# Performance work log

Measured on AMD Instinct MI355X. Metric: run time of the kernel, lower is better.

## Reference

```python
import jax, jax.numpy as jnp
import numpy as np

B, T, FEAT, H, E, NT, NH = 64, 256, 188, 512, 1024, 14, 8
HD = E // NH  # head dim = 128


def _gru_dir(x, w_ih, w_hh, b_ih, b_hh):
    # x: [T, B, in]; PyTorch GRU gate order: r, z, n
    xp = jnp.einsum('tbi,gi->tbg', x, w_ih) + b_ih  # [T,B,3H]

    def step(h, xt):
        hp = h @ w_hh.T + b_hh
        r = jax.nn.sigmoid(xt[..., :H] + hp[..., :H])
        z = jax.nn.sigmoid(xt[..., H:2 * H] + hp[..., H:2 * H])
        n = jnp.tanh(xt[..., 2 * H:] + r * hp[..., 2 * H:])
        h = (1 - z) * n + z * h
        return h, h

    h0 = jnp.zeros((x.shape[1], H), x.dtype)
    _, hs = jax.lax.scan(step, h0, xp)
    return hs  # [T,B,H]


def _bigru(x, wf, wb):
    f = _gru_dir(x, *wf)
    b = _gru_dir(x[::-1], *wb)[::-1]
    return jnp.concatenate([f, b], -1)  # [T,B,2H]


def _forward(features, ne_table, g1f, g1b, g2f, g2b, q_w, q_b, k_w, k_b, v_w, v_b,
             out_w, out_b, lin_w, lin_b, crf_start, crf_end, crf_trans, labels):
    nb = features.shape[0]
    x = features.transpose(1, 0, 2)  # [T,B,FEAT]
    enc = _bigru(x, g1f, g1b)        # [T,B,2H]=[T,B,E]
    # NE embedding: arange(14) rows for every batch element -> [S=14, B, 14]
    ne = jnp.broadcast_to(ne_table[:, None, :], (NT, nb, NT))
    # nn.MultiheadAttention with kdim=vdim=NT
    q = (enc @ q_w.T + q_b).reshape(T, nb, NH, HD)
    k = (ne @ k_w.T + k_b).reshape(NT, nb, NH, HD)
    v = (ne @ v_w.T + v_b).reshape(NT, nb, NH, HD)
    scores = jnp.einsum('tbhd,sbhd->bhts', q, k) / jnp.sqrt(jnp.float32(HD))
    attn = jax.nn.softmax(scores, axis=-1)
    ao = jnp.einsum('bhts,sbhd->tbhd', attn, v).reshape(T, nb, E)
    ao = ao @ out_w.T + out_b
    dec_in = jnp.concatenate([enc, ao], -1)   # [T,B,4H]
    dec = _bigru(dec_in, g2f, g2b)            # [T,B,2H]
    dec = dec @ lin_w.T + lin_b               # [T,B,NT]
    dec = dec.transpose(1, 0, 2)              # [B,T,NT]
    # scaled dot product against NE embeddings -> emissions [B,T,NT]
    logits = jnp.einsum('btd,sd->bts', dec, ne_table) / jnp.sqrt(jnp.float32(NT))
    # CRF negative log likelihood, reduction='mean', full mask
    em = jnp.take_along_axis(logits, labels[..., None], axis=2)[..., 0]  # [B,T]
    num = (crf_start[labels[:, 0]] + em.sum(1)
           + crf_trans[labels[:, :-1], labels[:, 1:]].sum(1)
           + crf_end[labels[:, -1]])
    alpha0 = crf_start + logits[:, 0]  # [B,NT]

    def step(a, e_t):
        a = jax.nn.logsumexp(a[:, :, None] + crf_trans[None] + e_t[:, None, :], axis=1)
        return a, None

    alpha, _ = jax.lax.scan(step, alpha0, logits[:, 1:].transpose(1, 0, 2))
    den = jax.nn.logsumexp(alpha + crf_end, axis=1)
    return -(num - den).mean()


def setup_inputs() -> dict:
    key = jax.random.key(0)
    ks = iter(jax.random.split(key, 40))

    def rn(shape, s=0.05):
        return jax.random.normal(next(ks), shape, jnp.float32) * s

    inp = {}
    inp['features'] = jax.random.normal(next(ks), (B, T, FEAT), jnp.float32)
    inp['labels'] = jax.random.randint(next(ks), (B, T), 0, NT)
    inp['ne_table'] = rn((NT, NT), 0.5).at[0].set(0.0)  # padding_idx=0
    for g, fi in (('gru1', FEAT), ('gru2', 4 * H)):
        for d in ('f', 'b'):
            inp[f'{g}_w_ih_{d}'] = rn((3 * H, fi))
            inp[f'{g}_w_hh_{d}'] = rn((3 * H, H))
            inp[f'{g}_b_ih_{d}'] = rn((3 * H,))
            inp[f'{g}_b_hh_{d}'] = rn((3 * H,))
    inp['q_w'] = rn((E, E)); inp['q_b'] = rn((E,))
    inp['k_w'] = rn((E, NT)); inp['k_b'] = rn((E,))
    inp['v_w'] = rn((E, NT)); inp['v_b'] = rn((E,))
    inp['out_w'] = rn((E, E)); inp['out_b'] = rn((E,))
    inp['lin_w'] = rn((NT, 2 * H)); inp['lin_b'] = rn((NT,))
    inp['crf_start'] = rn((NT,), 0.1)
    inp['crf_end'] = rn((NT,), 0.1)
    inp['crf_trans'] = rn((NT, NT), 0.1)
    return inp


def reference(features, labels, ne_table,
              gru1_w_ih_f, gru1_w_hh_f, gru1_b_ih_f, gru1_b_hh_f,
              gru1_w_ih_b, gru1_w_hh_b, gru1_b_ih_b, gru1_b_hh_b,
              gru2_w_ih_f, gru2_w_hh_f, gru2_b_ih_f, gru2_b_hh_f,
              gru2_w_ih_b, gru2_w_hh_b, gru2_b_ih_b, gru2_b_hh_b,
              q_w, q_b, k_w, k_b, v_w, v_b, out_w, out_b,
              lin_w, lin_b, crf_start, crf_end, crf_trans):
    return _forward(features, ne_table,
                    (gru1_w_ih_f, gru1_w_hh_f, gru1_b_ih_f, gru1_b_hh_f),
                    (gru1_w_ih_b, gru1_w_hh_b, gru1_b_ih_b, gru1_b_hh_b),
                    (gru2_w_ih_f, gru2_w_hh_f, gru2_b_ih_f, gru2_b_hh_f),
                    (gru2_w_ih_b, gru2_w_hh_b, gru2_b_ih_b, gru2_b_hh_b),
                    q_w, q_b, k_w, k_b, v_w, v_b, out_w, out_b,
                    lin_w, lin_b, crf_start, crf_end, crf_trans, labels)
```

## Files before the change

kernel.cpp:

```cpp
#include <hip/hip_runtime.h>
#include <hip/hip_bf16.h>
#include <math.h>

typedef __hip_bfloat16 bf16;
typedef __bf16 bf16x8 __attribute__((ext_vector_type(8)));
typedef float  f32x4  __attribute__((ext_vector_type(4)));
typedef unsigned long long u64;

#define T_SEQ 256
#define BATCH 64
#define FEATD 188
#define HID   512
#define EMB   1024
#define NTAG  14
#define G3    1536
#define GRU_NBLK 32
#define DIR_NBLK 16

__global__ __launch_bounds__(256) void f32_to_bf16(
    const float* __restrict__ src, bf16* __restrict__ dst, int n4)
{
  int i = blockIdx.x * 256 + threadIdx.x;
  if (i >= n4) return;
  float4 v = *(const float4*)(src + (size_t)i * 4);
  bf16 o[4] = {__float2bfloat16(v.x), __float2bfloat16(v.y),
               __float2bfloat16(v.z), __float2bfloat16(v.w)};
  *(ushort4*)(dst + (size_t)i * 4) = *(ushort4*)o;
}

__global__ __launch_bounds__(256) void gemm_mfma(
    const bf16* __restrict__ A1, int lda1,
    const bf16* __restrict__ A2, int lda2, int K1,
    const bf16* __restrict__ W, int ldw,
    const float* __restrict__ bias,
    bf16* __restrict__ C, int ldc,
    int M, int N, int K)
{
  __shared__ __bf16 As[128][40];
  __shared__ __bf16 Bs[128][40];
  const int bm = blockIdx.y * 128;
  const int bn = blockIdx.x * 128;
  const int tid = threadIdx.x;
  const int wave = tid >> 6, lane = tid & 63;
  const int wr = wave >> 1, wc = wave & 1;
  const int lr = lane & 15, lk = (lane >> 4) << 3;
  f32x4 acc[4][4] = {};
  for (int k0 = 0; k0 < K; k0 += 32) {
#pragma unroll
    for (int p = 0; p < 4; ++p) {
      int i = tid + p * 256;
      int row = i >> 3, q = i & 7;
      int kg = k0 + q * 4;
      ushort4 va{0, 0, 0, 0}, vb{0, 0, 0, 0};
      if (kg < K) {
        const bf16* srca = (kg < K1) ? A1 + (size_t)(bm + row) * lda1 + kg
                                     : A2 + (size_t)(bm + row) * lda2 + (kg - K1);
        va = *(const ushort4*)srca;
        vb = *(const ushort4*)(W + (size_t)(bn + row) * ldw + kg);
      }
      *(ushort4*)&As[row][q * 4] = va;
      *(ushort4*)&Bs[row][q * 4] = vb;
    }
    __syncthreads();
    bf16x8 af[4], bf_[4];
#pragma unroll
    for (int i = 0; i < 4; ++i)
      af[i] = *(const bf16x8*)&As[wr * 64 + i * 16 + lr][lk];
#pragma unroll
    for (int j = 0; j < 4; ++j)
      bf_[j] = *(const bf16x8*)&Bs[wc * 64 + j * 16 + lr][lk];
#pragma unroll
    for (int i = 0; i < 4; ++i)
#pragma unroll
      for (int j = 0; j < 4; ++j)
        acc[i][j] = __builtin_amdgcn_mfma_f32_16x16x32_bf16(af[i], bf_[j], acc[i][j], 0, 0, 0);
    __syncthreads();
  }
#pragma unroll
  for (int j = 0; j < 4; ++j) {
    int n = bn + wc * 64 + j * 16 + lr;
    float bv = bias ? bias[n] : 0.f;
#pragma unroll
    for (int i = 0; i < 4; ++i) {
#pragma unroll
      for (int p = 0; p < 4; ++p) {
        int m = bm + wr * 64 + i * 16 + (lane >> 4) * 4 + p;
        C[(size_t)m * ldc + n] = __float2bfloat16(acc[i][j][p] + bv);
      }
    }
  }
}

__global__ __launch_bounds__(256) void transpose_feat(
    const float* __restrict__ f, bf16* __restrict__ xT)
{
  const int idx = blockIdx.x * 256 + threadIdx.x;
  const int total = BATCH * T_SEQ * FEATD;
  if (idx >= total) return;
  const int i = idx % FEATD;
  const int r = idx / FEATD;
  const int b = r / T_SEQ;
  const int t = r % T_SEQ;
  xT[((size_t)t * BATCH + b) * FEATD + i] = __float2bfloat16(f[idx]);
}

__global__ __launch_bounds__(256, 1) void gru_persist(
    const bf16* __restrict__ xp_f, const bf16* __restrict__ xp_b,
    const bf16* __restrict__ whh_f, const bf16* __restrict__ whh_b,
    const float* __restrict__ bhh_f, const float* __restrict__ bhh_b,
    bf16* __restrict__ out, int* __restrict__ cnt)
{
  const int blk = blockIdx.x;
  const int dir = blk >> 4;
  const int ct  = blk & 15;
  const bf16* xp   = dir ? xp_b  : xp_f;
  const bf16* whh  = dir ? whh_b : whh_f;
  const float* bhh = dir ? bhh_b : bhh_f;
  const int off = dir ? HID : 0;
  const int tid = threadIdx.x;
  const int wave = tid >> 6, lane = tid & 63;
  const int lr = lane & 15, lkq = lane >> 4;
  int* mycnt = cnt + dir * T_SEQ;

  __shared__ __bf16 Ws[96][520];
  __shared__ __bf16 Hst[2][64][36];
  for (int i = tid; i < 96 * 64; i += 256) {
    int r = i >> 6, q = i & 63;
    int grow = (r >> 5) * HID + ct * 32 + (r & 31);
    *(float4*)&Ws[r][q * 8] = *(const float4*)(whh + (size_t)grow * HID + q * 8);
  }
  __syncthreads();

  float bh[3][2];
#pragma unroll
  for (int g = 0; g < 3; ++g)
#pragma unroll
    for (int nf = 0; nf < 2; ++nf)
      bh[g][nf] = bhh[g * HID + ct * 32 + nf * 16 + lr];

  bf16 xc[3][2][4];
  {
    const int t0 = dir ? (T_SEQ - 1) : 0;
    const size_t xbase = (size_t)t0 * BATCH * G3;
#pragma unroll
    for (int p = 0; p < 4; ++p) {
      const size_t xrow = xbase + (size_t)(wave * 16 + lkq * 4 + p) * G3;
#pragma unroll
      for (int g = 0; g < 3; ++g)
#pragma unroll
        for (int nf = 0; nf < 2; ++nf)
          xc[g][nf][p] = xp[xrow + g * HID + ct * 32 + nf * 16 + lr];
    }
  }

  for (int s = 0; s < T_SEQ; ++s) {
    const int t = dir ? (T_SEQ - 1 - s) : s;
    const int cur = s & 1, prv = cur ^ 1;

    f32x4 acc[3][2] = {};
    if (s > 0) {
      const bf16* arow = out + (size_t)(dir ? t + 1 : t - 1) * BATCH * EMB + off
                         + (size_t)(wave * 16 + lr) * EMB + lkq * 8;
      union { u64 v[2]; bf16x8 f; } hb[16];
#pragma unroll
      for (int ki = 0; ki < 16; ++ki) {
        hb[ki].v[0] = __hip_atomic_load((const u64*)(arow + ki * 32),
                                        __ATOMIC_RELAXED, __HIP_MEMORY_SCOPE_AGENT);
        hb[ki].v[1] = __hip_atomic_load((const u64*)(arow + ki * 32 + 4),
                                        __ATOMIC_RELAXED, __HIP_MEMORY_SCOPE_AGENT);
      }
#pragma unroll
      for (int ki = 0; ki < 16; ++ki) {
#pragma unroll
        for (int g = 0; g < 3; ++g)
#pragma unroll
          for (int nf = 0; nf < 2; ++nf) {
            bf16x8 b = *(const bf16x8*)&Ws[g * 32 + nf * 16 + lr][ki * 32 + lkq * 8];
            acc[g][nf] = __builtin_amdgcn_mfma_f32_16x16x32_bf16(hb[ki].f, b, acc[g][nf], 0, 0, 0);
          }
      }
    }

#pragma unroll
    for (int nf = 0; nf < 2; ++nf) {
      const int cl = nf * 16 + lr;
#pragma unroll
      for (int p = 0; p < 4; ++p) {
        const int m = wave * 16 + lkq * 4 + p;
        float hp = (s > 0) ? (float)Hst[prv][m][cl] : 0.f;
        float xr = __bfloat162float(xc[0][nf][p]);
        float xz = __bfloat162float(xc[1][nf][p]);
        float xn = __bfloat162float(xc[2][nf][p]);
        float r = 1.f / (1.f + expf(-(xr + acc[0][nf][p] + bh[0][nf])));
        float z = 1.f / (1.f + expf(-(xz + acc[1][nf][p] + bh[1][nf])));
        float n = tanhf(xn + r * (acc[2][nf][p] + bh[2][nf]));
        Hst[cur][m][cl] = (__bf16)((1.f - z) * n + z * hp);
      }
    }
    __syncthreads();

    const size_t obase = (size_t)t * BATCH * EMB + off + ct * 32;
    for (int i = tid; i < 512; i += 256) {
      int row = i >> 3, qq = i & 7;
      u64 v = *(const u64*)&Hst[cur][row][qq * 4];
      __hip_atomic_store((u64*)(out + obase + (size_t)row * EMB + qq * 4), v,
                         __ATOMIC_RELAXED, __HIP_MEMORY_SCOPE_AGENT);
    }
    asm volatile("s_waitcnt vmcnt(0)" ::: "memory");
    __syncthreads();

    if (tid == 0)
      __hip_atomic_fetch_add(&mycnt[s], 1, __ATOMIC_RELAXED, __HIP_MEMORY_SCOPE_AGENT);

    if (s + 1 < T_SEQ) {
      const int tn = dir ? (T_SEQ - 2 - s) : (s + 1);
      const size_t xb2 = (size_t)tn * BATCH * G3;
#pragma unroll
      for (int p = 0; p < 4; ++p) {
        const size_t xrow = xb2 + (size_t)(wave * 16 + lkq * 4 + p) * G3;
#pragma unroll
        for (int g = 0; g < 3; ++g)
#pragma unroll
          for (int nf = 0; nf < 2; ++nf)
            xc[g][nf][p] = xp[xrow + g * HID + ct * 32 + nf * 16 + lr];
      }
    }

    if (tid == 0) {
      while (__hip_atomic_load(&mycnt[s], __ATOMIC_RELAXED, __HIP_MEMORY_SCOPE_AGENT) < DIR_NBLK)
        __builtin_amdgcn_s_sleep(1);
    }
    __syncthreads();
  }
}

__global__ __launch_bounds__(256) void kv_kernel(
    const float* __restrict__ ne, const float* __restrict__ k_w,
    const float* __restrict__ k_b, const float* __restrict__ v_w,
    const float* __restrict__ v_b, float* __restrict__ kk,
    float* __restrict__ vv)
{
  const int e = blockIdx.x * 256 + threadIdx.x;
  if (e >= EMB) return;
#pragma unroll
  for (int s = 0; s < NTAG; ++s) {
    float a = k_b[e], c = v_b[e];
#pragma unroll
    for (int i = 0; i < NTAG; ++i) {
      float nv = ne[s * NTAG + i];
      a = fmaf(nv, k_w[e * NTAG + i], a);
      c = fmaf(nv, v_w[e * NTAG + i], c);
    }
    kk[s * EMB + e] = a;
    vv[s * EMB + e] = c;
  }
}

__global__ __launch_bounds__(256) void attn_kernel(
    const bf16* __restrict__ q, const float* __restrict__ kk,
    const float* __restrict__ vv, bf16* __restrict__ ao)
{
  const int unit = blockIdx.x * 4 + (threadIdx.x >> 6);
  const int h = unit & 7;
  const int tb = unit >> 3;
  const int lane = threadIdx.x & 63;
  const size_t qbase = (size_t)tb * EMB + h * 128;
  const int kbase = h * 128 + lane;
  float q0 = __bfloat162float(q[qbase + lane]);
  float q1 = __bfloat162float(q[qbase + 64 + lane]);
  float sc[NTAG];
#pragma unroll
  for (int j = 0; j < NTAG; ++j) {
    float p = q0 * kk[j * EMB + kbase] + q1 * kk[j * EMB + 64 + kbase];
#pragma unroll
    for (int d = 32; d; d >>= 1) p += __shfl_xor(p, d);
    sc[j] = p * 0.088388347648318447f;
  }
  float m = sc[0];
#pragma unroll
  for (int j = 1; j < NTAG; ++j) m = fmaxf(m, sc[j]);
  float sum = 0.f;
#pragma unroll
  for (int j = 0; j < NTAG; ++j) { sc[j] = expf(sc[j] - m); sum += sc[j]; }
  float inv = 1.f / sum;
  float o0 = 0.f, o1 = 0.f;
#pragma unroll
  for (int j = 0; j < NTAG; ++j) {
    float p = sc[j] * inv;
    o0 = fmaf(p, vv[j * EMB + kbase], o0);
    o1 = fmaf(p, vv[j * EMB + 64 + kbase], o1);
  }
  ao[qbase + lane] = __float2bfloat16(o0);
  ao[qbase + 64 + lane] = __float2bfloat16(o1);
}

__global__ __launch_bounds__(256) void dec_logits_kernel(
    const bf16* __restrict__ dec, const float* __restrict__ lin_w,
    const float* __restrict__ lin_b, const float* __restrict__ ne,
    float* __restrict__ logits)
{
  const int tb = blockIdx.x * 4 + (threadIdx.x >> 6);
  const int t = tb >> 6;
  const int b = tb & 63;
  const int lane = threadIdx.x & 63;
  const bf16* drow = dec + (size_t)tb * EMB;
  float dv[16];
#pragma unroll
  for (int i = 0; i < 16; ++i) dv[i] = __bfloat162float(drow[lane + 64 * i]);
  float dl[NTAG];
#pragma unroll
  for (int n = 0; n < NTAG; ++n) {
    float p = 0.f;
#pragma unroll
    for (int i = 0; i < 16; ++i)
      p = fmaf(dv[i], lin_w[n * EMB + lane + 64 * i], p);
#pragma unroll
    for (int d = 32; d; d >>= 1) p += __shfl_xor(p, d);
    dl[n] = p + lin_b[n];
  }
  if (lane < NTAG) {
    float acc = 0.f;
#pragma unroll
    for (int d2 = 0; d2 < NTAG; ++d2)
      acc = fmaf(dl[d2], ne[lane * NTAG + d2], acc);
    logits[((size_t)b * T_SEQ + t) * NTAG + lane] = acc * 0.26726124191242439f;
  }
}

__global__ __launch_bounds__(64) void crf_kernel(
    const float* __restrict__ logits, const int* __restrict__ labels,
    const float* __restrict__ cstart, const float* __restrict__ cend,
    const float* __restrict__ ctrans, float* __restrict__ lossb)
{
  const int b = blockIdx.x;
  const int lane = threadIdx.x;
  __shared__ float al[NTAG];
  __shared__ float tr[NTAG * NTAG];
  __shared__ float tmp[NTAG];
  const float* lg = logits + (size_t)b * T_SEQ * NTAG;
  const int* lab = labels + (size_t)b * T_SEQ;
  for (int i = lane; i < NTAG * NTAG; i += 64) tr[i] = ctrans[i];
  if (lane < NTAG) al[lane] = cstart[lane] + lg[lane];
  __syncthreads();
  for (int t = 1; t < T_SEQ; ++t) {
    float v = 0.f;
    if (lane < NTAG) {
      float mx = -1e30f;
#pragma unroll
      for (int i = 0; i < NTAG; ++i) mx = fmaxf(mx, al[i] + tr[i * NTAG + lane]);
      float sm = 0.f;
#pragma unroll
      for (int i = 0; i < NTAG; ++i) sm += expf(al[i] + tr[i * NTAG + lane] - mx);
      v = mx + logf(sm) + lg[t * NTAG + lane];
    }
    __syncthreads();
    if (lane < NTAG) al[lane] = v;
    __syncthreads();
  }
  float em = 0.f;
  for (int t = lane; t < T_SEQ; t += 64) em += lg[t * NTAG + lab[t]];
  float trs = 0.f;
  for (int t = lane; t < T_SEQ - 1; t += 64) trs += tr[lab[t] * NTAG + lab[t + 1]];
  float p = em + trs;
#pragma unroll
  for (int d = 32; d; d >>= 1) p += __shfl_xor(p, d);
  if (lane < NTAG) tmp[lane] = al[lane] + cend[lane];
  __syncthreads();
  if (lane == 0) {
    float num = p + cstart[lab[0]] + cend[lab[T_SEQ - 1]];
    float mx = tmp[0];
#pragma unroll
    for (int i = 1; i < NTAG; ++i) mx = fmaxf(mx, tmp[i]);
    float sm = 0.f;
#pragma unroll
    for (int i = 0; i < NTAG; ++i) sm += expf(tmp[i] - mx);
    float den = mx + logf(sm);
    lossb[b] = -(num - den);
  }
}

__global__ __launch_bounds__(64) void final_reduce(
    const float* __restrict__ lossb, float* __restrict__ out)
{
  float v = lossb[threadIdx.x];
#pragma unroll
  for (int d = 32; d; d >>= 1) v += __shfl_xor(v, d);
  if (threadIdx.x == 0) out[0] = v * (1.f / 64.f);
}

extern "C" void kernel_launch(void* const* d_in, const int* in_sizes, int n_in,
                              void* d_out, int out_size, void* d_ws, size_t ws_size,
                              hipStream_t stream)
{
  const float* features = (const float*)d_in[0];
  const int*   labels   = (const int*)d_in[1];
  const float* ne_table = (const float*)d_in[2];
  const float* g1_wih_f = (const float*)d_in[3];
  const float* g1_whh_f = (const float*)d_in[4];
  const float* g1_bih_f = (const float*)d_in[5];
  const float* g1_bhh_f = (const float*)d_in[6];
  const float* g1_wih_b = (const float*)d_in[7];
  const float* g1_whh_b = (const float*)d_in[8];
  const float* g1_bih_b = (const float*)d_in[9];
  const float* g1_bhh_b = (const float*)d_in[10];
  const float* g2_wih_f = (const float*)d_in[11];
  const float* g2_whh_f = (const float*)d_in[12];
  const float* g2_bih_f = (const float*)d_in[13];
  const float* g2_bhh_f = (const float*)d_in[14];
  const float* g2_wih_b = (const float*)d_in[15];
  const float* g2_whh_b = (const float*)d_in[16];
  const float* g2_bih_b = (const float*)d_in[17];
  const float* g2_bhh_b = (const float*)d_in[18];
  const float* q_w   = (const float*)d_in[19];
  const float* q_b   = (const float*)d_in[20];
  const float* k_w   = (const float*)d_in[21];
  const float* k_b   = (const float*)d_in[22];
  const float* v_w   = (const float*)d_in[23];
  const float* v_b   = (const float*)d_in[24];
  const float* out_w = (const float*)d_in[25];
  const float* out_b = (const float*)d_in[26];
  const float* lin_w = (const float*)d_in[27];
  const float* lin_b = (const float*)d_in[28];
  const float* crf_start = (const float*)d_in[29];
  const float* crf_end   = (const float*)d_in[30];
  const float* crf_trans = (const float*)d_in[31];

  const size_t NTB = (size_t)T_SEQ * BATCH;
  char* base = (char*)d_ws;
  size_t off = 0;
  auto alloc = [&](size_t bytes) {
    char* p = base + off;
    off += (bytes + 255) & ~(size_t)255;
    return p;
  };
  bf16* xpA  = (bf16*)alloc(NTB * G3 * sizeof(bf16));
  bf16* xpB  = (bf16*)alloc(NTB * G3 * sizeof(bf16));
  bf16* enc  = (bf16*)alloc(NTB * EMB * sizeof(bf16));
  bf16* bufD = (bf16*)alloc(NTB * EMB * sizeof(bf16));
  bf16* bufE = (bf16*)alloc(NTB * EMB * sizeof(bf16));
  float* kkbuf  = (float*)alloc((size_t)NTAG * EMB * sizeof(float));
  float* vvbuf  = (float*)alloc((size_t)NTAG * EMB * sizeof(float));
  float* logits = (float*)alloc(NTB * NTAG * sizeof(float));
  float* lossb  = (float*)alloc(64 * sizeof(float));
  int*   bcnt   = (int*)alloc(1024 * sizeof(int));
  bf16* w1if = (bf16*)alloc((size_t)G3 * FEATD * sizeof(bf16));
  bf16* w1ib = (bf16*)alloc((size_t)G3 * FEATD * sizeof(bf16));
  bf16* w1hf = (bf16*)alloc((size_t)G3 * HID * sizeof(bf16));
  bf16* w1hb = (bf16*)alloc((size_t)G3 * HID * sizeof(bf16));
  bf16* w2if = (bf16*)alloc((size_t)G3 * 2 * EMB * sizeof(bf16));
  bf16* w2ib = (bf16*)alloc((size_t)G3 * 2 * EMB * sizeof(bf16));
  bf16* w2hf = (bf16*)alloc((size_t)G3 * HID * sizeof(bf16));
  bf16* w2hb = (bf16*)alloc((size_t)G3 * HID * sizeof(bf16));
  bf16* wq   = (bf16*)alloc((size_t)EMB * EMB * sizeof(bf16));
  bf16* wo   = (bf16*)alloc((size_t)EMB * EMB * sizeof(bf16));
  (void)off; (void)ws_size; (void)in_sizes; (void)n_in; (void)out_size;

  bf16* xT = bufD;

  const int M = (int)NTB;
  dim3 blk(256);

  hipMemsetAsync(bcnt, 0, 1024 * sizeof(int), stream);

  auto conv = [&](const float* s, bf16* d, size_t n) {
    f32_to_bf16<<<(int)((n / 4 + 255) / 256), blk, 0, stream>>>(s, d, (int)(n / 4));
  };
  conv(g1_wih_f, w1if, (size_t)G3 * FEATD);
  conv(g1_wih_b, w1ib, (size_t)G3 * FEATD);
  conv(g1_whh_f, w1hf, (size_t)G3 * HID);
  conv(g1_whh_b, w1hb, (size_t)G3 * HID);
  conv(g2_wih_f, w2if, (size_t)G3 * 2 * EMB);
  conv(g2_wih_b, w2ib, (size_t)G3 * 2 * EMB);
  conv(g2_whh_f, w2hf, (size_t)G3 * HID);
  conv(g2_whh_b, w2hb, (size_t)G3 * HID);
  conv(q_w, wq, (size_t)EMB * EMB);
  conv(out_w, wo, (size_t)EMB * EMB);

  transpose_feat<<<(BATCH * T_SEQ * FEATD + 255) / 256, blk, 0, stream>>>(features, xT);

  dim3 g_xp(G3 / 128, M / 128);
  dim3 g_e(EMB / 128, M / 128);

  gemm_mfma<<<g_xp, blk, 0, stream>>>(xT, FEATD, nullptr, 0, FEATD,
                                      w1if, FEATD, g1_bih_f, xpA, G3, M, G3, FEATD);
  gemm_mfma<<<g_xp, blk, 0, stream>>>(xT, FEATD, nullptr, 0, FEATD,
                                      w1ib, FEATD, g1_bih_b, xpB, G3, M, G3, FEATD);

  gru_persist<<<GRU_NBLK, blk, 0, stream>>>(xpA, xpB, w1hf, w1hb,
                                            g1_bhh_f, g1_bhh_b, enc, bcnt);

  kv_kernel<<<4, blk, 0, stream>>>(ne_table, k_w, k_b, v_w, v_b, kkbuf, vvbuf);
  gemm_mfma<<<g_e, blk, 0, stream>>>(enc, EMB, nullptr, 0, EMB,
                                     wq, EMB, q_b, bufE, EMB, M, EMB, EMB);

  attn_kernel<<<M * 2, blk, 0, stream>>>(bufE, kkbuf, vvbuf, bufD);
  gemm_mfma<<<g_e, blk, 0, stream>>>(bufD, EMB, nullptr, 0, EMB,
                                     wo, EMB, out_b, bufE, EMB, M, EMB, EMB);

  gemm_mfma<<<g_xp, blk, 0, stream>>>(enc, EMB, bufE, EMB, EMB,
                                      w2if, 2 * EMB, g2_bih_f, xpA, G3, M, G3, 2 * EMB);
  gemm_mfma<<<g_xp, blk, 0, stream>>>(enc, EMB, bufE, EMB, EMB,
                                      w2ib, 2 * EMB, g2_bih_b, xpB, G3, M, G3, 2 * EMB);

  gru_persist<<<GRU_NBLK, blk, 0, stream>>>(xpA, xpB, w2hf, w2hb,
                                            g2_bhh_f, g2_bhh_b, bufD, bcnt + 512);

  dec_logits_kernel<<<M / 4, blk, 0, stream>>>(bufD, lin_w, lin_b, ne_table, logits);

  crf_kernel<<<BATCH, 64, 0, stream>>>(logits, labels, crf_start, crf_end, crf_trans, lossb);
  final_reduce<<<1, 64, 0, stream>>>(lossb, (float*)d_out);
}
```

Before: 5.042 ms.

## Restructure persistent GRU: register-resident weights, fewer blocks, per-block flag barrier

The persistent GRU kernel now runs 8 blocks per direction instead of 16, and each wave keeps its slice of the recurrent weights in registers rather than LDS. Each step stages the full previous hidden state into swizzled LDS and computes 64 gate columns per block. The hidden state stays in fp32 registers, and outputs are written as packed bf16 pairs straight from the accumulators. The old atomic counter barrier, polled by one thread followed by __syncthreads, is replaced by per-block ready flags that a whole wave polls. This shortens the inter-block synchronisation latency on the serial recurrence, at the cost of heavy register pressure and half as many CUs doing the per-step work.

```diff
diff --git a/kernel.cpp b/kernel.cpp
--- a/kernel.cpp
+++ b/kernel.cpp
@@ -14,8 +14,9 @@
 #define EMB   1024
 #define NTAG  14
 #define G3    1536
-#define GRU_NBLK 32
-#define DIR_NBLK 16
+#define GRU_NBLK 16
+#define DIR_NBLK 8
+#define FLAG_REGION (T_SEQ * 16 * 2)
 
 __global__ __launch_bounds__(256) void f32_to_bf16(
     const float* __restrict__ src, bf16* __restrict__ dst, int n4)
@@ -108,11 +109,11 @@
     const bf16* __restrict__ xp_f, const bf16* __restrict__ xp_b,
     const bf16* __restrict__ whh_f, const bf16* __restrict__ whh_b,
     const float* __restrict__ bhh_f, const float* __restrict__ bhh_b,
-    bf16* __restrict__ out, int* __restrict__ cnt)
+    bf16* __restrict__ out, int* __restrict__ flags)
 {
   const int blk = blockIdx.x;
-  const int dir = blk >> 4;
-  const int ct  = blk & 15;
+  const int dir = blk >> 3;
+  const int ct  = blk & 7;
   const bf16* xp   = dir ? xp_b  : xp_f;
   const bf16* whh  = dir ? whh_b : whh_f;
   const float* bhh = dir ? bhh_b : bhh_f;
@@ -120,117 +121,138 @@
   const int tid = threadIdx.x;
   const int wave = tid >> 6, lane = tid & 63;
   const int lr = lane & 15, lkq = lane >> 4;
-  int* mycnt = cnt + dir * T_SEQ;
-
-  __shared__ __bf16 Ws[96][520];
-  __shared__ __bf16 Hst[2][64][36];
-  for (int i = tid; i < 96 * 64; i += 256) {
-    int r = i >> 6, q = i & 63;
-    int grow = (r >> 5) * HID + ct * 32 + (r & 31);
-    *(float4*)&Ws[r][q * 8] = *(const float4*)(whh + (size_t)grow * HID + q * 8);
-  }
-  __syncthreads();
-
-  float bh[3][2];
+  const int c = ct * 64 + wave * 16 + lr;
+  int* fl = flags + dir * (T_SEQ * 16);
+
+  __shared__ u64 hlbuf[8192];
+  char* hl = (char*)hlbuf;
+
+  bf16x8 wreg[3][16];
 #pragma unroll
   for (int g = 0; g < 3; ++g)
 #pragma unroll
-    for (int nf = 0; nf < 2; ++nf)
-      bh[g][nf] = bhh[g * HID + ct * 32 + nf * 16 + lr];
-
-  bf16 xc[3][2][4];
+    for (int ki = 0; ki < 16; ++ki)
+      wreg[g][ki] = *(const bf16x8*)(whh + (size_t)(g * HID + c) * HID + ki * 32 + lkq * 8);
+
+  float bh[3];
+#pragma unroll
+  for (int g = 0; g < 3; ++g) bh[g] = bhh[g * HID + c];
+
+  float hp[4][4] = {};
+
+  bf16 xc[3][4][4];
   {
     const int t0 = dir ? (T_SEQ - 1) : 0;
-    const size_t xbase = (size_t)t0 * BATCH * G3;
-#pragma unroll
-    for (int p = 0; p < 4; ++p) {
-      const size_t xrow = xbase + (size_t)(wave * 16 + lkq * 4 + p) * G3;
-#pragma unroll
-      for (int g = 0; g < 3; ++g)
-#pragma unroll
-        for (int nf = 0; nf < 2; ++nf)
-          xc[g][nf][p] = xp[xrow + g * HID + ct * 32 + nf * 16 + lr];
-    }
+    const size_t xb = (size_t)t0 * BATCH * G3;
+#pragma unroll
+    for (int mi = 0; mi < 4; ++mi)
+#pragma unroll
+      for (int p = 0; p < 4; ++p) {
+        const size_t xrow = xb + (size_t)(mi * 16 + lkq * 4 + p) * G3;
+#pragma unroll
+        for (int g = 0; g < 3; ++g)
+          xc[g][mi][p] = xp[xrow + g * HID + c];
+      }
   }
 
   for (int s = 0; s < T_SEQ; ++s) {
     const int t = dir ? (T_SEQ - 1 - s) : s;
-    const int cur = s & 1, prv = cur ^ 1;
-
-    f32x4 acc[3][2] = {};
+
+    f32x4 acc[3][4] = {};
     if (s > 0) {
-      const bf16* arow = out + (size_t)(dir ? t + 1 : t - 1) * BATCH * EMB + off
-                         + (size_t)(wave * 16 + lr) * EMB + lkq * 8;
-      union { u64 v[2]; bf16x8 f; } hb[16];
+      const int tp = dir ? t + 1 : t - 1;
+      const bf16* hsrc = out + (size_t)tp * BATCH * EMB + off;
+      u64 hv[32];
+#pragma unroll
+      for (int it = 0; it < 32; ++it) {
+        int slot = it * 256 + tid;
+        int row = slot >> 7;
+        int colel = (slot << 2) & 511;
+        hv[it] = __hip_atomic_load((const u64*)(hsrc + (size_t)row * EMB + colel),
+                                   __ATOMIC_RELAXED, __HIP_MEMORY_SCOPE_AGENT);
+      }
+#pragma unroll
+      for (int it = 0; it < 32; ++it) {
+        int slot = it * 256 + tid;
+        int row = slot >> 7;
+        int lb = (row << 10) + (((slot << 2) & 511) << 1);
+        lb ^= (row & 7) << 4;
+        *(u64*)(hl + lb) = hv[it];
+      }
+      __syncthreads();
 #pragma unroll
       for (int ki = 0; ki < 16; ++ki) {
-        hb[ki].v[0] = __hip_atomic_load((const u64*)(arow + ki * 32),
-                                        __ATOMIC_RELAXED, __HIP_MEMORY_SCOPE_AGENT);
-        hb[ki].v[1] = __hip_atomic_load((const u64*)(arow + ki * 32 + 4),
-                                        __ATOMIC_RELAXED, __HIP_MEMORY_SCOPE_AGENT);
-      }
-#pragma unroll
-      for (int ki = 0; ki < 16; ++ki) {
+        bf16x8 a[4];
+#pragma unroll
+        for (int mi = 0; mi < 4; ++mi) {
+          int row = mi * 16 + lr;
+          int ab = (row << 10) + ki * 64 + lkq * 16;
+          ab ^= (row & 7) << 4;
+          a[mi] = *(const bf16x8*)(hl + ab);
+        }
 #pragma unroll
         for (int g = 0; g < 3; ++g)
 #pragma unroll
-          for (int nf = 0; nf < 2; ++nf) {
-            bf16x8 b = *(const bf16x8*)&Ws[g * 32 + nf * 16 + lr][ki * 32 + lkq * 8];
-            acc[g][nf] = __builtin_amdgcn_mfma_f32_16x16x32_bf16(hb[ki].f, b, acc[g][nf], 0, 0, 0);
-          }
-      }
+          for (int mi = 0; mi < 4; ++mi)
+            acc[g][mi] = __builtin_amdgcn_mfma_f32_16x16x32_bf16(a[mi], wreg[g][ki], acc[g][mi], 0, 0, 0);
+      }
+      __syncthreads();
     }
 
-#pragma unroll
-    for (int nf = 0; nf < 2; ++nf) {
-      const int cl = nf * 16 + lr;
+    const size_t obase = (size_t)t * BATCH * EMB + off;
+#pragma unroll
+    for (int mi = 0; mi < 4; ++mi)
 #pragma unroll
       for (int p = 0; p < 4; ++p) {
-        const int m = wave * 16 + lkq * 4 + p;
-        float hp = (s > 0) ? (float)Hst[prv][m][cl] : 0.f;
-        float xr = __bfloat162float(xc[0][nf][p]);
-        float xz = __bfloat162float(xc[1][nf][p]);
-        float xn = __bfloat162float(xc[2][nf][p]);
-        float r = 1.f / (1.f + expf(-(xr + acc[0][nf][p] + bh[0][nf])));
-        float z = 1.f / (1.f + expf(-(xz + acc[1][nf][p] + bh[1][nf])));
-        float n = tanhf(xn + r * (acc[2][nf][p] + bh[2][nf]));
-        Hst[cur][m][cl] = (__bf16)((1.f - z) * n + z * hp);
-      }
-    }
-    __syncthreads();
-
-    const size_t obase = (size_t)t * BATCH * EMB + off + ct * 32;
-    for (int i = tid; i < 512; i += 256) {
-      int row = i >> 3, qq = i & 7;
-      u64 v = *(const u64*)&Hst[cur][row][qq * 4];
-      __hip_atomic_store((u64*)(out + obase + (size_t)row * EMB + qq * 4), v,
-                         __ATOMIC_RELAXED, __HIP_MEMORY_SCOPE_AGENT);
-    }
-    asm volatile("s_waitcnt vmcnt(0)" ::: "memory");
-    __syncthreads();
-
-    if (tid == 0)
-      __hip_atomic_fetch_add(&mycnt[s], 1, __ATOMIC_RELAXED, __HIP_MEMORY_SCOPE_AGENT);
+        const int m = mi * 16 + lkq * 4 + p;
+        float xr = __bfloat162float(xc[0][mi][p]);
+        float xz = __bfloat162float(xc[1][mi][p]);
+        float xn = __bfloat162float(xc[2][mi][p]);
+        float r = 1.f / (1.f + expf(-(xr + acc[0][mi][p] + bh[0])));
+        float z = 1.f / (1.f + expf(-(xz + acc[1][mi][p] + bh[1])));
+        float n = tanhf(xn + r * (acc[2][mi][p] + bh[2]));
+        float h = (1.f - z) * n + z * hp[mi][p];
+        hp[mi][p] = h;
+        bf16 hvb = __float2bfloat16(h);
+        int mb = *(unsigned short*)&hvb;
+        int pb = __shfl_xor(mb, 1);
+        if (!(lr & 1)) {
+          unsigned int pk = (unsigned int)mb | ((unsigned int)pb << 16);
+          __hip_atomic_store((unsigned int*)(out + obase + (size_t)m * EMB + c), pk,
+                             __ATOMIC_RELAXED, __HIP_MEMORY_SCOPE_AGENT);
+        }
+      }
 
     if (s + 1 < T_SEQ) {
+      asm volatile("s_waitcnt vmcnt(0)" ::: "memory");
+      __syncthreads();
+      if (tid == 0)
+        __hip_atomic_store(&fl[s * 16 + ct], 1,
+                           __ATOMIC_RELAXED, __HIP_MEMORY_SCOPE_AGENT);
       const int tn = dir ? (T_SEQ - 2 - s) : (s + 1);
       const size_t xb2 = (size_t)tn * BATCH * G3;
 #pragma unroll
-      for (int p = 0; p < 4; ++p) {
-        const size_t xrow = xb2 + (size_t)(wave * 16 + lkq * 4 + p) * G3;
-#pragma unroll
-        for (int g = 0; g < 3; ++g)
-#pragma unroll
-          for (int nf = 0; nf < 2; ++nf)
-            xc[g][nf][p] = xp[xrow + g * HID + ct * 32 + nf * 16 + lr];
-      }
+      for (int mi = 0; mi < 4; ++mi)
+#pragma unroll
+        for (int p = 0; p < 4; ++p) {
+          const size_t xrow = xb2 + (size_t)(mi * 16 + lkq * 4 + p) * G3;
+#pragma unroll
+          for (int g = 0; g < 3; ++g)
+            xc[g][mi][p] = xp[xrow + g * HID + c];
+        }
+      __builtin_amdgcn_sched_barrier(0);
+      int ready = 0;
+      do {
+        int f = 1;
+        if (lane < DIR_NBLK)
+          f = __hip_atomic_load(&fl[s * 16 + lane],
+                                __ATOMIC_RELAXED, __HIP_MEMORY_SCOPE_AGENT);
+        ready = __all(f != 0);
+        if (!ready) __builtin_amdgcn_s_sleep(1);
+      } while (!ready);
+    } else {
+      asm volatile("s_waitcnt vmcnt(0)" ::: "memory");
     }
-
-    if (tid == 0) {
-      while (__hip_atomic_load(&mycnt[s], __ATOMIC_RELAXED, __HIP_MEMORY_SCOPE_AGENT) < DIR_NBLK)
-        __builtin_amdgcn_s_sleep(1);
-    }
-    __syncthreads();
   }
 }
 
@@ -442,7 +464,7 @@
   float* vvbuf  = (float*)alloc((size_t)NTAG * EMB * sizeof(float));
   float* logits = (float*)alloc(NTB * NTAG * sizeof(float));
   float* lossb  = (float*)alloc(64 * sizeof(float));
-  int*   bcnt   = (int*)alloc(1024 * sizeof(int));
+  int*   flags  = (int*)alloc(2 * FLAG_REGION * sizeof(int));
   bf16* w1if = (bf16*)alloc((size_t)G3 * FEATD * sizeof(bf16));
   bf16* w1ib = (bf16*)alloc((size_t)G3 * FEATD * sizeof(bf16));
   bf16* w1hf = (bf16*)alloc((size_t)G3 * HID * sizeof(bf16));
@@ -460,7 +482,7 @@
   const int M = (int)NTB;
   dim3 blk(256);
 
-  hipMemsetAsync(bcnt, 0, 1024 * sizeof(int), stream);
+  hipMemsetAsync(flags, 0, 2 * FLAG_REGION * sizeof(int), stream);
 
   auto conv = [&](const float* s, bf16* d, size_t n) {
     f32_to_bf16<<<(int)((n / 4 + 255) / 256), blk, 0, stream>>>(s, d, (int)(n / 4));
@@ -487,7 +509,7 @@
                                       w1ib, FEATD, g1_bih_b, xpB, G3, M, G3, FEATD);
 
   gru_persist<<<GRU_NBLK, blk, 0, stream>>>(xpA, xpB, w1hf, w1hb,
-                                            g1_bhh_f, g1_bhh_b, enc, bcnt);
+                                            g1_bhh_f, g1_bhh_b, enc, flags);
 
   kv_kernel<<<4, blk, 0, stream>>>(ne_table, k_w, k_b, v_w, v_b, kkbuf, vvbuf);
   gemm_mfma<<<g_e, blk, 0, stream>>>(enc, EMB, nullptr, 0, EMB,
@@ -503,7 +525,8 @@
                                       w2ib, 2 * EMB, g2_bih_b, xpB, G3, M, G3, 2 * EMB);
 
   gru_persist<<<GRU_NBLK, blk, 0, stream>>>(xpA, xpB, w2hf, w2hb,
-                                            g2_bhh_f, g2_bhh_b, bufD, bcnt + 512);
+                                            g2_bhh_f, g2_bhh_b, bufD,
+                                            flags + FLAG_REGION);
 
   dec_logits_kernel<<<M / 4, blk, 0, stream>>>(bufD, lin_w, lin_b, ne_table, logits);
 
```

Result: slower. 7.660 ms (+51.9%).
